# Kernel tuning notes

Hardware: AMD Instinct MI355X
Metric: run time of the kernel (lower is better)

The kernel has to match this reference:

```python
import jax, jax.numpy as jnp
import numpy as np

EPS = 1e-5
DIM_HEAD = 64
HEADS = 16
SCALE = DIM_HEAD ** -0.5


def rotate_half(x):
    # '... (j d) -> ... j d' with j=2, then (-x2, x1)
    x = x.reshape(*x.shape[:-1], 2, x.shape[-1] // 2)
    x1, x2 = x[..., 0, :], x[..., 1, :]
    return jnp.concatenate((-x2, x1), axis=-1)


def apply_rotary(freqs, t):
    # freqs: (n, rot_dim) broadcasts against t: (b, h, n, d)
    rot_dim = freqs.shape[-1]
    t_rot, t_pass = t[..., :rot_dim], t[..., rot_dim:]
    t_rot = t_rot * jnp.cos(freqs) + rotate_half(t_rot) * jnp.sin(freqs)
    return jnp.concatenate((t_rot, t_pass), axis=-1)


def setup_inputs() -> dict:
    key = jax.random.key(0)
    ks = jax.random.split(key, 4)
    b, n, dim = 2, 2048, 1024
    inner = HEADS * DIM_HEAD
    x = jax.random.normal(ks[0], (b, n, dim), dtype=jnp.float32)
    mask = jnp.ones((b, n), dtype=bool)
    rotary_pos_emb = jax.random.normal(ks[1], (n, 32), dtype=jnp.float32)
    W_qkv = jax.random.normal(ks[2], (dim, inner * 3), dtype=jnp.float32) * (dim ** -0.5)
    W_out = jax.random.normal(ks[3], (inner, dim), dtype=jnp.float32) * (inner ** -0.5)
    gamma = jnp.ones((dim,), dtype=jnp.float32)
    return {"x": x, "mask": mask, "rotary_pos_emb": rotary_pos_emb,
            "W_qkv": W_qkv, "W_out": W_out, "gamma": gamma}


def reference(x, mask, rotary_pos_emb, W_qkv, W_out, gamma):
    b, n, _ = x.shape
    qkv = x @ W_qkv  # (b, n, 3*inner)
    q, k, v = jnp.split(qkv, 3, axis=-1)
    def split_heads(t):
        return t.reshape(b, n, HEADS, DIM_HEAD).transpose(0, 2, 1, 3)  # b h n d
    q, k, v = map(split_heads, (q, k, v))
    q = q * SCALE
    q = apply_rotary(rotary_pos_emb, q)
    k = apply_rotary(rotary_pos_emb, k)
    v = apply_rotary(rotary_pos_emb, v)
    sim = jnp.einsum('bhid,bhjd->bhij', q, k)
    mask_value = -jnp.finfo(sim.dtype).max
    sim = jnp.where(mask[:, None, None, :], sim, mask_value)
    sim = sim - jax.lax.stop_gradient(jnp.max(sim, axis=-1, keepdims=True))
    attn = jax.nn.softmax(sim, axis=-1)
    out = jnp.einsum('bhij,bhjd->bhid', attn, v)
    out = out.transpose(0, 2, 1, 3).reshape(b, n, HEADS * DIM_HEAD)
    out = out @ W_out
    # LayerNorm with learned gamma, zero beta
    mean = jnp.mean(out, axis=-1, keepdims=True)
    var = jnp.var(out, axis=-1, keepdims=True)
    out = (out - mean) * jax.lax.rsqrt(var + EPS) * gamma
    return out
```

## Files before the change

### kernel.cpp

```cpp
#include <hip/hip_runtime.h>

typedef __attribute__((ext_vector_type(8))) short s16x8;
typedef __attribute__((ext_vector_type(4))) float f32x4;

#define AS1q __attribute__((address_space(1)))
#define AS3q __attribute__((address_space(3)))

__device__ __forceinline__ void gload16(const void* g, void* l) {
  __builtin_amdgcn_global_load_lds((const AS1q unsigned int*)g,
                                   (AS3q unsigned int*)l, 16, 0, 0);
}

__device__ __forceinline__ unsigned short f2bf(float f) {
  unsigned int u = __float_as_uint(f);
  u = (u + 0x7FFFu + ((u >> 16) & 1u)) >> 16;
  return (unsigned short)u;
}

__device__ __forceinline__ unsigned int cvtpk(float a, float b) {
  unsigned int r;
  asm("v_cvt_pk_bf16_f32 %0, %1, %2" : "=v"(r) : "v"(a), "v"(b));
  return r;
}

__global__ void trig_kernel(const float* __restrict__ rope,
                            float* __restrict__ cosT, float* __restrict__ sinT) {
  int i = blockIdx.x * 256 + threadIdx.x;
  float f = rope[i];
  cosT[i] = cosf(f);
  sinT[i] = sinf(f);
}

__global__ void cast_kernel(const float* __restrict__ in, unsigned short* __restrict__ out) {
  int i = (blockIdx.x * 256 + threadIdx.x) * 4;
  float4 v = *(const float4*)(in + i);
  ushort4 o;
  o.x = f2bf(v.x); o.y = f2bf(v.y); o.z = f2bf(v.z); o.w = f2bf(v.w);
  *(ushort4*)(out + i) = o;
}

__global__ __launch_bounds__(256) void tcast_kernel(const float* __restrict__ in,
    unsigned short* __restrict__ out, int K, int N) {
  __shared__ float tile[32][33];
  int k0 = blockIdx.x * 32, n0 = blockIdx.y * 32;
  int tx = threadIdx.x & 31, ty = threadIdx.x >> 5;
  #pragma unroll
  for (int r = ty; r < 32; r += 8) tile[r][tx] = in[(size_t)(k0 + r) * N + n0 + tx];
  __syncthreads();
  #pragma unroll
  for (int r = ty; r < 32; r += 8) out[(size_t)(n0 + r) * K + k0 + tx] = f2bf(tile[tx][r]);
}

__global__ __launch_bounds__(256) void gemm_bt(
    const unsigned short* __restrict__ A, const unsigned short* __restrict__ Bt,
    float* __restrict__ C, int M, int N, int K) {
  __shared__ alignas(16) unsigned short Al[128 * 64];
  __shared__ alignas(16) unsigned short Bl[128 * 64];
  int tid = threadIdx.x, w = tid >> 6, l = tid & 63;
  int l16 = l & 15, lg = l >> 4;
  int m0 = blockIdx.x * 128, n0 = blockIdx.y * 128;
  f32x4 acc[4][4] = {};
  int srow0 = w * 8 + (l >> 3);
  int sblk = l & 7;
  for (int k0 = 0; k0 < K; k0 += 64) {
    __syncthreads();
    #pragma unroll
    for (int c = 0; c < 4; c++) {
      int row = c * 32 + srow0;
      gload16((const char*)A + ((size_t)(m0 + row) * K + k0) * 2 + ((sblk ^ (row & 7)) * 16),
              (char*)Al + c * 4096 + w * 1024);
      gload16((const char*)Bt + ((size_t)(n0 + row) * K + k0) * 2 + ((sblk ^ (row & 7)) * 16),
              (char*)Bl + c * 4096 + w * 1024);
    }
    __syncthreads();
    #pragma unroll
    for (int kk = 0; kk < 2; kk++) {
      s16x8 af[4], bf[4];
      #pragma unroll
      for (int i = 0; i < 4; i++) {
        int ar = (w >> 1) * 64 + i * 16 + l16;
        int ab = ar * 128 + (kk * 32 + 8 * lg) * 2; ab ^= (ar & 7) << 4;
        af[i] = *(const s16x8*)((const char*)Al + ab);
        int br = (w & 1) * 64 + i * 16 + l16;
        int bb = br * 128 + (kk * 32 + 8 * lg) * 2; bb ^= (br & 7) << 4;
        bf[i] = *(const s16x8*)((const char*)Bl + bb);
      }
      #pragma unroll
      for (int i = 0; i < 4; i++)
        #pragma unroll
        for (int j = 0; j < 4; j++)
          acc[i][j] = __builtin_amdgcn_mfma_f32_16x16x32_bf16(af[i], bf[j], acc[i][j], 0, 0, 0);
    }
  }
  #pragma unroll
  for (int i = 0; i < 4; i++)
    #pragma unroll
    for (int j = 0; j < 4; j++)
      #pragma unroll
      for (int r = 0; r < 4; r++) {
        int mrow = m0 + (w >> 1) * 64 + i * 16 + 4 * lg + r;
        int ncol = n0 + (w & 1) * 64 + j * 16 + l16;
        C[(size_t)mrow * N + ncol] = acc[i][j][r];
      }
}

__global__ __launch_bounds__(256) void gemm_qkv(
    const unsigned short* __restrict__ A, const unsigned short* __restrict__ Bt,
    const float* __restrict__ cosT, const float* __restrict__ sinT,
    unsigned short* __restrict__ Qb, unsigned short* __restrict__ Kb,
    unsigned short* __restrict__ Vb, int K) {
  __shared__ alignas(16) char smem[34816];
  unsigned short* Al = (unsigned short*)smem;
  unsigned short* Bl = Al + 128 * 64;
  float (*cs)[68] = (float(*)[68])smem;
  int tid = threadIdx.x, w = tid >> 6, l = tid & 63;
  int l16 = l & 15, lg = l >> 4;
  int m0 = blockIdx.x * 128, n0 = blockIdx.y * 128;
  f32x4 acc[4][4] = {};
  int srow0 = w * 8 + (l >> 3);
  int sblk = l & 7;
  for (int k0 = 0; k0 < K; k0 += 64) {
    __syncthreads();
    #pragma unroll
    for (int c = 0; c < 4; c++) {
      int row = c * 32 + srow0;
      gload16((const char*)A + ((size_t)(m0 + row) * K + k0) * 2 + ((sblk ^ (row & 7)) * 16),
              (char*)Al + c * 4096 + w * 1024);
      gload16((const char*)Bt + ((size_t)(n0 + row) * K + k0) * 2 + ((sblk ^ (row & 7)) * 16),
              (char*)Bl + c * 4096 + w * 1024);
    }
    __syncthreads();
    #pragma unroll
    for (int kk = 0; kk < 2; kk++) {
      s16x8 af[4], bf[4];
      #pragma unroll
      for (int i = 0; i < 4; i++) {
        int ar = (w >> 1) * 64 + i * 16 + l16;
        int ab = ar * 128 + (kk * 32 + 8 * lg) * 2; ab ^= (ar & 7) << 4;
        af[i] = *(const s16x8*)((const char*)Al + ab);
        int br = (w & 1) * 64 + i * 16 + l16;
        int bb = br * 128 + (kk * 32 + 8 * lg) * 2; bb ^= (br & 7) << 4;
        bf[i] = *(const s16x8*)((const char*)Bl + bb);
      }
      #pragma unroll
      for (int i = 0; i < 4; i++)
        #pragma unroll
        for (int j = 0; j < 4; j++)
          acc[i][j] = __builtin_amdgcn_mfma_f32_16x16x32_bf16(af[i], bf[j], acc[i][j], 0, 0, 0);
    }
  }
  __syncthreads();
  int b = m0 >> 11;
  int nnb = m0 & 2047;
  for (int g = tid; g < 128 * 16; g += 256) {
    int row = g >> 4;
    int c4 = (g & 15) * 4;
    float4 val;
    if (c4 < 32) val = *(const float4*)(cosT + (size_t)(nnb + row) * 32 + c4);
    else         val = *(const float4*)(sinT + (size_t)(nnb + row) * 32 + (c4 - 32));
    *(float4*)&cs[row][c4] = val;
  }
  __syncthreads();
  int section = n0 >> 10;
  int h = ((n0 & 1023) >> 6) + (w & 1);
  unsigned short* dst = section == 0 ? Qb : (section == 1 ? Kb : Vb);
  float scl = section == 0 ? 0.18033688011112042f : 1.0f;
  #pragma unroll
  for (int i = 0; i < 4; i++)
    #pragma unroll
    for (int r = 0; r < 4; r++) {
      int lrow = (w >> 1) * 64 + i * 16 + 4 * lg + r;
      float c0 = cs[lrow][l16],      s0 = cs[lrow][32 + l16];
      float c1 = cs[lrow][16 + l16], s1 = cs[lrow][48 + l16];
      float a0 = acc[i][0][r], a1 = acc[i][1][r];
      float o0 = (c0 * a0 - s0 * a1) * scl;
      float o1 = (c1 * a1 + s1 * a0) * scl;
      float o2 = acc[i][2][r] * scl;
      float o3 = acc[i][3][r] * scl;
      int nn = nnb + lrow;
      size_t obase = ((size_t)(b * 16 + h) * 2048 + nn) * 64;
      dst[obase + l16]      = f2bf(o0);
      dst[obase + 16 + l16] = f2bf(o1);
      dst[obase + 32 + l16] = f2bf(o2);
      dst[obase + 48 + l16] = f2bf(o3);
    }
}

__global__ __launch_bounds__(256) void vtrans_kernel(const unsigned short* __restrict__ Vb,
                                                     unsigned short* __restrict__ Vt) {
  __shared__ unsigned short vt[64][65];
  int nb = blockIdx.x, bh = blockIdx.y;
  int t = threadIdx.x;
  int nl = t >> 2, quarter = t & 3;
  size_t src = ((size_t)bh * 2048 + nb * 64 + nl) * 64 + quarter * 16;
  s16x8 v0 = *(const s16x8*)(Vb + src);
  s16x8 v1 = *(const s16x8*)(Vb + src + 8);
  #pragma unroll
  for (int i = 0; i < 8; i++) {
    vt[nl][quarter * 16 + i] = (unsigned short)v0[i];
    vt[nl][quarter * 16 + 8 + i] = (unsigned short)v1[i];
  }
  __syncthreads();
  int drow = t >> 2;
  size_t dstb = ((size_t)bh * 64 + drow) * 2048 + (size_t)nb * 64 + (size_t)quarter * 16;
  s16x8 o0, o1;
  #pragma unroll
  for (int j = 0; j < 8; j++) {
    int p = quarter * 16 + j;
    int c = 32 * (p >> 5) + 16 * ((p >> 2) & 1) + 4 * ((p >> 3) & 3) + (p & 3);
    o0[j] = (short)vt[c][drow];
  }
  #pragma unroll
  for (int j = 0; j < 8; j++) {
    int p = quarter * 16 + 8 + j;
    int c = 32 * (p >> 5) + 16 * ((p >> 2) & 1) + 4 * ((p >> 3) & 3) + (p & 3);
    o1[j] = (short)vt[c][drow];
  }
  *(s16x8*)(Vt + dstb) = o0;
  *(s16x8*)(Vt + dstb + 8) = o1;
}

__global__ __launch_bounds__(256) void flash_kernel(
    const unsigned short* __restrict__ Q, const unsigned short* __restrict__ K,
    const unsigned short* __restrict__ Vt, unsigned short* __restrict__ A2) {
  __shared__ alignas(16) unsigned short Kl[2][64 * 64];
  __shared__ alignas(16) unsigned short Vl[2][64 * 64];
  int id = blockIdx.x;
  int s = id >> 3;
  int bh = (id & 7) * 4 + (s >> 4);
  int qblk = s & 15;
  int tid = threadIdx.x, w = tid >> 6, l = tid & 63;
  int l16 = l & 15, lg = l >> 4;
  size_t base = (size_t)bh * 2048 * 64;
  const unsigned short* Qb = Q + base;
  const unsigned short* Kb = K + base;
  const unsigned short* Vb = Vt + base;
  int q0 = qblk * 128 + w * 16;
  s16x8 qfA[2], qfB[2];
  {
    const s16x8* qpA = (const s16x8*)(Qb + (size_t)(q0 + l16) * 64);
    qfA[0] = qpA[lg]; qfA[1] = qpA[lg + 4];
    const s16x8* qpB = (const s16x8*)(Qb + (size_t)(q0 + 64 + l16) * 64);
    qfB[0] = qpB[lg]; qfB[1] = qpB[lg + 4];
  }
  float lsumA = 0.f, lsumB = 0.f;
  f32x4 oA[4], oB[4];
  #pragma unroll
  for (int nd = 0; nd < 4; nd++) {
    f32x4 z = {0.f, 0.f, 0.f, 0.f};
    oA[nd] = z; oB[nd] = z;
  }
  int srow0 = w * 8 + (l >> 3);
  int sblk = l & 7;
  auto STAGE = [&](int buf, int t0) {
    #pragma unroll
    for (int c = 0; c < 2; c++) {
      int row = c * 32 + srow0;
      gload16((const char*)Kb + (size_t)(t0 + row) * 128 + ((sblk ^ (row & 7)) * 16),
              (char*)Kl[buf] + c * 4096 + w * 1024);
      gload16((const char*)Vb + (size_t)row * 4096 + (size_t)t0 * 2 + ((sblk ^ (row & 7)) * 16),
              (char*)Vl[buf] + c * 4096 + w * 1024);
    }
  };
  STAGE(0, 0);
  __syncthreads();
  int cur = 0;
  for (int t0 = 0; t0 < 2048; t0 += 64) {
    if (t0 + 64 < 2048) STAGE(cur ^ 1, t0 + 64);
    const char* Kc = (const char*)Kl[cur];
    const char* Vc = (const char*)Vl[cur];
    f32x4 sfA[4], sfB[4];
    #pragma unroll
    for (int nbt = 0; nbt < 4; nbt++) {
      f32x4 z = {0.f, 0.f, 0.f, 0.f};
      sfA[nbt] = z; sfB[nbt] = z;
      #pragma unroll
      for (int kk = 0; kk < 2; kk++) {
        int kvrow = nbt * 16 + l16;
        int byte_ = kvrow * 128 + (kk * 32 + 8 * lg) * 2;
        byte_ ^= (kvrow & 7) << 4;
        s16x8 bfr = *(const s16x8*)(Kc + byte_);
        sfA[nbt] = __builtin_amdgcn_mfma_f32_16x16x32_bf16(bfr, qfA[kk], sfA[nbt], 0, 0, 0);
        sfB[nbt] = __builtin_amdgcn_mfma_f32_16x16x32_bf16(bfr, qfB[kk], sfB[nbt], 0, 0, 0);
      }
    }
    s16x8 paA0, paA1, paB0, paB1;
    {
      float e0[4], e1[4], e2[4], e3[4];
      #pragma unroll
      for (int r = 0; r < 4; r++) {
        e0[r] = __builtin_amdgcn_exp2f(sfA[0][r]);
        e1[r] = __builtin_amdgcn_exp2f(sfA[1][r]);
        e2[r] = __builtin_amdgcn_exp2f(sfA[2][r]);
        e3[r] = __builtin_amdgcn_exp2f(sfA[3][r]);
      }
      lsumA += ((e0[0] + e0[1]) + (e0[2] + e0[3])) + ((e1[0] + e1[1]) + (e1[2] + e1[3]))
             + ((e2[0] + e2[1]) + (e2[2] + e2[3])) + ((e3[0] + e3[1]) + (e3[2] + e3[3]));
      unsigned int* w0 = (unsigned int*)&paA0;
      unsigned int* w1 = (unsigned int*)&paA1;
      w0[0] = cvtpk(e0[0], e0[1]); w0[1] = cvtpk(e0[2], e0[3]);
      w0[2] = cvtpk(e1[0], e1[1]); w0[3] = cvtpk(e1[2], e1[3]);
      w1[0] = cvtpk(e2[0], e2[1]); w1[1] = cvtpk(e2[2], e2[3]);
      w1[2] = cvtpk(e3[0], e3[1]); w1[3] = cvtpk(e3[2], e3[3]);
    }
    {
      float e0[4], e1[4], e2[4], e3[4];
      #pragma unroll
      for (int r = 0; r < 4; r++) {
        e0[r] = __builtin_amdgcn_exp2f(sfB[0][r]);
        e1[r] = __builtin_amdgcn_exp2f(sfB[1][r]);
        e2[r] = __builtin_amdgcn_exp2f(sfB[2][r]);
        e3[r] = __builtin_amdgcn_exp2f(sfB[3][r]);
      }
      lsumB += ((e0[0] + e0[1]) + (e0[2] + e0[3])) + ((e1[0] + e1[1]) + (e1[2] + e1[3]))
             + ((e2[0] + e2[1]) + (e2[2] + e2[3])) + ((e3[0] + e3[1]) + (e3[2] + e3[3]));
      unsigned int* w0 = (unsigned int*)&paB0;
      unsigned int* w1 = (unsigned int*)&paB1;
      w0[0] = cvtpk(e0[0], e0[1]); w0[1] = cvtpk(e0[2], e0[3]);
      w0[2] = cvtpk(e1[0], e1[1]); w0[3] = cvtpk(e1[2], e1[3]);
      w1[0] = cvtpk(e2[0], e2[1]); w1[1] = cvtpk(e2[2], e2[3]);
      w1[2] = cvtpk(e3[0], e3[1]); w1[3] = cvtpk(e3[2], e3[3]);
    }
    #pragma unroll
    for (int nk = 0; nk < 2; nk++) {
      s16x8 pA = nk ? paA1 : paA0;
      s16x8 pB = nk ? paB1 : paB0;
      #pragma unroll
      for (int nd = 0; nd < 4; nd++) {
        int drow = nd * 16 + l16;
        int vb = drow * 128 + (nk * 32 + 8 * lg) * 2;
        vb ^= (drow & 7) << 4;
        s16x8 vfr = *(const s16x8*)(Vc + vb);
        oA[nd] = __builtin_amdgcn_mfma_f32_16x16x32_bf16(pA, vfr, oA[nd], 0, 0, 0);
        oB[nd] = __builtin_amdgcn_mfma_f32_16x16x32_bf16(pB, vfr, oB[nd], 0, 0, 0);
      }
    }
    __syncthreads();
    cur ^= 1;
  }
  float sA = lsumA, sB = lsumB;
  sA += __shfl_xor(sA, 16); sA += __shfl_xor(sA, 32);
  sB += __shfl_xor(sB, 16); sB += __shfl_xor(sB, 32);
  float rsA[4], rsB[4];
  #pragma unroll
  for (int r = 0; r < 4; r++) {
    rsA[r] = __builtin_amdgcn_rcpf(__shfl(sA, 4 * lg + r));
    rsB[r] = __builtin_amdgcn_rcpf(__shfl(sB, 4 * lg + r));
  }
  int b = bh >> 4, h = bh & 15;
  #pragma unroll
  for (int nd = 0; nd < 4; nd++)
    #pragma unroll
    for (int r = 0; r < 4; r++) {
      int qA = q0 + 4 * lg + r;
      int d = nd * 16 + l16;
      A2[((size_t)(b * 2048 + qA)) * 1024 + h * 64 + d] = f2bf(oA[nd][r] * rsA[r]);
      A2[((size_t)(b * 2048 + qA + 64)) * 1024 + h * 64 + d] = f2bf(oB[nd][r] * rsB[r]);
    }
}

__global__ __launch_bounds__(256) void ln_kernel(const float* __restrict__ in,
    const float* __restrict__ gamma, float* __restrict__ out) {
  __shared__ float red[8];
  int row = blockIdx.x, t = threadIdx.x;
  const float* r = in + (size_t)row * 1024;
  float4 v = *(const float4*)(r + t * 4);
  float s = v.x + v.y + v.z + v.w;
  float s2 = v.x * v.x + v.y * v.y + v.z * v.z + v.w * v.w;
  #pragma unroll
  for (int off = 1; off < 64; off <<= 1) { s += __shfl_xor(s, off); s2 += __shfl_xor(s2, off); }
  if ((t & 63) == 0) { red[t >> 6] = s; red[4 + (t >> 6)] = s2; }
  __syncthreads();
  float S = red[0] + red[1] + red[2] + red[3];
  float S2 = red[4] + red[5] + red[6] + red[7];
  float mean = S * (1.f / 1024.f);
  float var = S2 * (1.f / 1024.f) - mean * mean;
  float inv = rsqrtf(var + 1e-5f);
  float4 g = *(const float4*)(gamma + t * 4);
  float4 ov;
  ov.x = (v.x - mean) * inv * g.x;
  ov.y = (v.y - mean) * inv * g.y;
  ov.z = (v.z - mean) * inv * g.z;
  ov.w = (v.w - mean) * inv * g.w;
  *(float4*)(out + (size_t)row * 1024 + t * 4) = ov;
}

extern "C" void kernel_launch(void* const* d_in, const int* in_sizes, int n_in,
                              void* d_out, int out_size, void* d_ws, size_t ws_size,
                              hipStream_t stream) {
  const float* x     = (const float*)d_in[0];
  const float* rope  = (const float*)d_in[2];
  const float* Wqkv  = (const float*)d_in[3];
  const float* Wout  = (const float*)d_in[4];
  const float* gamma = (const float*)d_in[5];
  float* out = (float*)d_out;

  char* ws = (char*)d_ws;
  unsigned short* Qb  = (unsigned short*)(ws + 0);
  unsigned short* Kb  = (unsigned short*)(ws + 8388608);
  unsigned short* Vb  = (unsigned short*)(ws + 16777216);
  unsigned short* Vt  = (unsigned short*)(ws + 25165824);
  float*          out2= (float*)(ws + 33554432);
  unsigned short* xb  = (unsigned short*)(ws + 50331648);
  unsigned short* wqT = (unsigned short*)(ws + 58720256);
  unsigned short* woT = (unsigned short*)(ws + 65011712);
  float*          cosT= (float*)(ws + 67108864);
  float*          sinT= (float*)(ws + 67371008);
  unsigned short* a2 = xb;

  trig_kernel<<<256, 256, 0, stream>>>(rope, cosT, sinT);
  cast_kernel<<<4096, 256, 0, stream>>>(x, xb);
  tcast_kernel<<<dim3(32, 96), 256, 0, stream>>>(Wqkv, wqT, 1024, 3072);
  tcast_kernel<<<dim3(32, 32), 256, 0, stream>>>(Wout, woT, 1024, 1024);
  gemm_qkv<<<dim3(32, 24), 256, 0, stream>>>(xb, wqT, cosT, sinT, Qb, Kb, Vb, 1024);
  vtrans_kernel<<<dim3(32, 32), 256, 0, stream>>>(Vb, Vt);
  flash_kernel<<<512, 256, 0, stream>>>(Qb, Kb, Vt, a2);
  gemm_bt<<<dim3(32, 8), 256, 0, stream>>>(a2, woT, out2, 4096, 1024, 1024);
  ln_kernel<<<4096, 256, 0, stream>>>(out2, gamma, out);
}
```

Before: 142.1 us.

## Double-buffer LDS tiles in QKV and output GEMMs to overlap loads with MFMA

Both GEMM kernels now keep two LDS buffers for the A and B tiles. The next K-tile is loaded with global_load_lds while MFMAs run on the current one, which drops one of the two barriers per iteration. The aim is to hide global load latency behind compute. In exchange LDS use per block doubles (about 64KB), which can lower occupancy. The loop relies on a single barrier at its end, which must cover both completion of the async loads and the LDS read-after-write hazard.

```diff
diff --git a/kernel.cpp b/kernel.cpp
--- a/kernel.cpp
+++ b/kernel.cpp
@@ -54,25 +54,31 @@
 __global__ __launch_bounds__(256) void gemm_bt(
     const unsigned short* __restrict__ A, const unsigned short* __restrict__ Bt,
     float* __restrict__ C, int M, int N, int K) {
-  __shared__ alignas(16) unsigned short Al[128 * 64];
-  __shared__ alignas(16) unsigned short Bl[128 * 64];
+  __shared__ alignas(16) unsigned short Al[2][128 * 64];
+  __shared__ alignas(16) unsigned short Bl[2][128 * 64];
   int tid = threadIdx.x, w = tid >> 6, l = tid & 63;
   int l16 = l & 15, lg = l >> 4;
   int m0 = blockIdx.x * 128, n0 = blockIdx.y * 128;
   f32x4 acc[4][4] = {};
   int srow0 = w * 8 + (l >> 3);
   int sblk = l & 7;
-  for (int k0 = 0; k0 < K; k0 += 64) {
-    __syncthreads();
+  auto STAGE = [&](int buf, int k0) {
     #pragma unroll
     for (int c = 0; c < 4; c++) {
       int row = c * 32 + srow0;
       gload16((const char*)A + ((size_t)(m0 + row) * K + k0) * 2 + ((sblk ^ (row & 7)) * 16),
-              (char*)Al + c * 4096 + w * 1024);
+              (char*)Al[buf] + c * 4096 + w * 1024);
       gload16((const char*)Bt + ((size_t)(n0 + row) * K + k0) * 2 + ((sblk ^ (row & 7)) * 16),
-              (char*)Bl + c * 4096 + w * 1024);
-    }
-    __syncthreads();
+              (char*)Bl[buf] + c * 4096 + w * 1024);
+    }
+  };
+  STAGE(0, 0);
+  __syncthreads();
+  int cur = 0;
+  for (int k0 = 0; k0 < K; k0 += 64) {
+    if (k0 + 64 < K) STAGE(cur ^ 1, k0 + 64);
+    const char* Ac = (const char*)Al[cur];
+    const char* Bc = (const char*)Bl[cur];
     #pragma unroll
     for (int kk = 0; kk < 2; kk++) {
       s16x8 af[4], bf[4];
@@ -80,10 +86,10 @@
       for (int i = 0; i < 4; i++) {
         int ar = (w >> 1) * 64 + i * 16 + l16;
         int ab = ar * 128 + (kk * 32 + 8 * lg) * 2; ab ^= (ar & 7) << 4;
-        af[i] = *(const s16x8*)((const char*)Al + ab);
+        af[i] = *(const s16x8*)(Ac + ab);
         int br = (w & 1) * 64 + i * 16 + l16;
         int bb = br * 128 + (kk * 32 + 8 * lg) * 2; bb ^= (br & 7) << 4;
-        bf[i] = *(const s16x8*)((const char*)Bl + bb);
+        bf[i] = *(const s16x8*)(Bc + bb);
       }
       #pragma unroll
       for (int i = 0; i < 4; i++)
@@ -91,6 +97,8 @@
         for (int j = 0; j < 4; j++)
           acc[i][j] = __builtin_amdgcn_mfma_f32_16x16x32_bf16(af[i], bf[j], acc[i][j], 0, 0, 0);
     }
+    __syncthreads();
+    cur ^= 1;
   }
   #pragma unroll
   for (int i = 0; i < 4; i++)
@@ -109,9 +117,7 @@
     const float* __restrict__ cosT, const float* __restrict__ sinT,
     unsigned short* __restrict__ Qb, unsigned short* __restrict__ Kb,
     unsigned short* __restrict__ Vb, int K) {
-  __shared__ alignas(16) char smem[34816];
-  unsigned short* Al = (unsigned short*)smem;
-  unsigned short* Bl = Al + 128 * 64;
+  __shared__ alignas(16) char smem[65536];
   float (*cs)[68] = (float(*)[68])smem;
   int tid = threadIdx.x, w = tid >> 6, l = tid & 63;
   int l16 = l & 15, lg = l >> 4;
@@ -119,17 +125,25 @@
   f32x4 acc[4][4] = {};
   int srow0 = w * 8 + (l >> 3);
   int sblk = l & 7;
-  for (int k0 = 0; k0 < K; k0 += 64) {
-    __syncthreads();
+  auto STAGE = [&](int buf, int k0) {
+    char* Ad = smem + buf * 16384;
+    char* Bd = smem + 32768 + buf * 16384;
     #pragma unroll
     for (int c = 0; c < 4; c++) {
       int row = c * 32 + srow0;
       gload16((const char*)A + ((size_t)(m0 + row) * K + k0) * 2 + ((sblk ^ (row & 7)) * 16),
-              (char*)Al + c * 4096 + w * 1024);
+              Ad + c * 4096 + w * 1024);
       gload16((const char*)Bt + ((size_t)(n0 + row) * K + k0) * 2 + ((sblk ^ (row & 7)) * 16),
-              (char*)Bl + c * 4096 + w * 1024);
-    }
-    __syncthreads();
+              Bd + c * 4096 + w * 1024);
+    }
+  };
+  STAGE(0, 0);
+  __syncthreads();
+  int cur = 0;
+  for (int k0 = 0; k0 < K; k0 += 64) {
+    if (k0 + 64 < K) STAGE(cur ^ 1, k0 + 64);
+    const char* Ac = smem + cur * 16384;
+    const char* Bc = smem + 32768 + cur * 16384;
     #pragma unroll
     for (int kk = 0; kk < 2; kk++) {
       s16x8 af[4], bf[4];
@@ -137,10 +151,10 @@
       for (int i = 0; i < 4; i++) {
         int ar = (w >> 1) * 64 + i * 16 + l16;
         int ab = ar * 128 + (kk * 32 + 8 * lg) * 2; ab ^= (ar & 7) << 4;
-        af[i] = *(const s16x8*)((const char*)Al + ab);
+        af[i] = *(const s16x8*)(Ac + ab);
         int br = (w & 1) * 64 + i * 16 + l16;
         int bb = br * 128 + (kk * 32 + 8 * lg) * 2; bb ^= (br & 7) << 4;
-        bf[i] = *(const s16x8*)((const char*)Bl + bb);
+        bf[i] = *(const s16x8*)(Bc + bb);
       }
       #pragma unroll
       for (int i = 0; i < 4; i++)
@@ -148,8 +162,9 @@
         for (int j = 0; j < 4; j++)
           acc[i][j] = __builtin_amdgcn_mfma_f32_16x16x32_bf16(af[i], bf[j], acc[i][j], 0, 0, 0);
     }
-  }
-  __syncthreads();
+    __syncthreads();
+    cur ^= 1;
+  }
   int b = m0 >> 11;
   int nnb = m0 & 2047;
   for (int g = tid; g < 128 * 16; g += 256) {
```

New measurement: 128.3 us. 9.7% less time.
